# Kernel tuning notes

Measured on AMD Instinct MI355X. Metric: run time of the kernel, lower is better.

## Reference

```python
import jax, jax.numpy as jnp
import numpy as np

B, S, D, H, G, K = 4, 4096, 1024, 16, 4, 3
DG = D // G   # group channels = 256
DH = D // H   # head channels = 64


def setup_inputs() -> dict:
    key = jax.random.key(0)
    ks = jax.random.split(key, 8)
    def w(k, shape, std=0.02):
        return jax.random.normal(k, shape, jnp.float32) * std
    return {
        "x": jax.random.normal(ks[0], (B, S, D), jnp.float32),
        "Wq": w(ks[1], (D, D)), "bq": jnp.zeros((D,), jnp.float32),
        "Wk": w(ks[2], (D, D)), "bk": jnp.zeros((D,), jnp.float32),
        "Wv": w(ks[3], (D, D)), "bv": jnp.zeros((D,), jnp.float32),
        "Wo": w(ks[4], (D, D)), "bo": jnp.zeros((D,), jnp.float32),
        "Woff1": w(ks[5], (DG, DG, K)), "boff1": jnp.zeros((DG,), jnp.float32),
        "Woff2": w(ks[6], (DG,)),
        "bias_table": w(ks[7], (1, 1, S)),
    }


def reference(x, Wq, bq, Wk, bk, Wv, bv, Wo, bo, Woff1, boff1, Woff2, bias_table):
    bsz, seq, d = x.shape
    scale = d ** (-0.5)
    xc = jnp.transpose(x, (0, 2, 1))  # [B, D, S]

    # 1x1 conv projections == channel GEMMs
    q = jnp.einsum('oc,bcs->bos', Wq, xc) + bq[None, :, None]  # [B, D, S]

    # group: [B*G, DG, S]
    gq = q.reshape(bsz * G, DG, seq)
    # offset head: conv1d(k=3, pad=1) -> conv1d(k=1, no bias) -> [B*G, S]
    h = jax.lax.conv_general_dilated(
        gq, Woff1, window_strides=(1,), padding=((K // 2, K // 2),),
        dimension_numbers=('NCH', 'OIH', 'NCH')) + boff1[None, :, None]
    offset = jnp.einsum('c,bcs->bs', Woff2, h)
    offset = jnp.tanh(offset) * K  # offset_range_factor = kernel

    gx = xc.reshape(bsz * G, DG, seq)  # grouped x

    # faithful replication of _grid_sample_1d: F.grid_sample on feats [N,C,S,1]
    # with grid (x = vgrid_scaled -> width dim of size 1, y = 0 -> height dim of
    # size S), bilinear, zero padding, align_corners=False.
    grid = jnp.arange(seq, dtype=x.dtype)[None, :]
    vgrid_scaled = 2.0 * (grid + offset) / max(seq - 1, 1) - 1.0  # [B*G, S]
    ix = vgrid_scaled / 2.0                 # unnormalized width coord (W=1)
    wx = jnp.clip(1.0 - jnp.abs(ix), 0.0, 1.0)  # bilinear weight on width idx 0
    iy = (seq - 1) / 2.0                    # unnormalized height coord for y=0
    y0 = int(np.floor(iy)); y1 = min(y0 + 1, seq - 1)
    wy1 = float(iy - y0); wy0 = 1.0 - wy1
    feat_c = wy0 * gx[:, :, y0] + wy1 * gx[:, :, y1]  # [B*G, DG]
    x_sampled = feat_c[:, :, None] * wx[:, None, :]   # [B*G, DG, S]
    xs = x_sampled.reshape(bsz, d, seq)               # ungroup -> [B, D, S]

    k = jnp.einsum('oc,bcs->bos', Wk, xs) + bk[None, :, None]
    v = jnp.einsum('oc,bcs->bos', Wv, xs) + bv[None, :, None]

    qh = q.reshape(bsz * H, DH, seq)
    kh = k.reshape(bsz * H, DH, seq)
    vh = v.reshape(bsz * H, DH, seq) + bias_table[:, :, :seq]

    # channel attention: contract over sequence dim (as in the original einsum)
    scores = jnp.einsum('bis,bjs->bij', qh, kh) * scale  # [B*H, DH, DH]
    attn = jax.nn.softmax(scores, axis=-1)
    out = jnp.einsum('bij,bjs->bis', attn, vh)           # [B*H, DH, S]
    out = out.reshape(bsz, d, seq).transpose(0, 2, 1)     # [B, S, D]
    return jnp.einsum('bsd,od->bso', out, Wo) + bo
```

## Files before the change

kernel.cpp:

```cpp
#include <hip/hip_runtime.h>
#include <math.h>

#define BB 4
#define SS 4096
#define DD 1024
#define HH 16
#define GG 4
#define KK 3
#define DG 256
#define DH 64
#define CH 32
#define NCH (SS / CH)

enum : size_t {
  OFF_WEFF  = 0,
  OFF_OFFC  = 1024,
  OFF_WEQ   = 1280,
  OFF_WX    = 13568,
  OFF_XWP   = 79104,
  OFF_XW    = 2700544,
  OFF_XS    = 2716928,
  OFF_SW    = 2721024,
  OFF_FEAT  = 2721280,
  OFF_KF    = 2725376,
  OFF_VF    = 2741760,
  OFF_QW    = 2758144,
  OFF_QS    = 2774528,
  OFF_AV    = 2778624,
  OFF_AB    = 2795008,
  OFF_C2    = 2799104,
  OFF_WAV   = 2803200,
  OFF_WOSUM = 2819584,
  WS_FLOATS = 2820608
};

__device__ __forceinline__ float wred_sum(float v) {
#pragma unroll
  for (int o = 32; o > 0; o >>= 1) v += __shfl_xor(v, o, 64);
  return v;
}
__device__ __forceinline__ float wred_max(float v) {
#pragma unroll
  for (int o = 32; o > 0; o >>= 1) v = fmaxf(v, __shfl_xor(v, o, 64));
  return v;
}

__global__ void k_pre1(const float* __restrict__ Woff1, const float* __restrict__ Woff2,
                       const float* __restrict__ x, const float* __restrict__ Wo,
                       float* __restrict__ ws) {
  const int t = threadIdx.x;
  const int lane = t & 63;
  if (blockIdx.x < 192) {
    const int widx = (blockIdx.x * 256 + t) >> 6;
    const int i = widx / 3, kk = widx - 3 * i;
    float a = 0.f;
#pragma unroll
    for (int u = 0; u < 4; ++u) {
      const int cc = lane + 64 * u;
      a += Woff2[cc] * Woff1[(size_t)(cc * DG + i) * KK + kk];
    }
    a = wred_sum(a);
    if (lane == 0) ws[OFF_WEFF + widx] = a;
  } else if (blockIdx.x < 208) {
    const int gid = (blockIdx.x - 192) * 256 + t;
    const int b = gid >> 10, c = gid & 1023;
    ws[OFF_FEAT + gid] = 0.5f * (x[((size_t)b * SS + 2047) * DD + c] +
                                 x[((size_t)b * SS + 2048) * DD + c]);
  } else {
    const int o = ((blockIdx.x - 208) * 256 + t) >> 6;
    const float4* wo = (const float4*)(Wo + (size_t)o * DD);
    float v = 0.f;
#pragma unroll
    for (int it = 0; it < 4; ++it) {
      const float4 a = wo[lane + 64 * it];
      v += a.x + a.y + a.z + a.w;
    }
    v = wred_sum(v);
    if (lane == 0) ws[OFF_WOSUM + o] = v;
  }
}

__global__ void k_pre2(const float* __restrict__ Wq, const float* __restrict__ bq,
                       const float* __restrict__ Woff2, const float* __restrict__ boff1,
                       float* __restrict__ ws) {
  const float* Weff = ws + OFF_WEFF;
  const int t = threadIdx.x;
  const int lane = t & 63;
  if (blockIdx.x < 192) {
    const int j = blockIdx.x >> 4;
    const int c0 = (blockIdx.x & 15) * 64;
    const int g = j / 3, kk = j - 3 * g;
    const int q = t >> 6;
    float a = 0.f;
#pragma unroll 4
    for (int ii = 0; ii < 64; ++ii) {
      const int i = q * 64 + ii;
      a += Weff[i * KK + kk] * Wq[(size_t)(g * DG + i) * DD + c0 + lane];
    }
    __shared__ float red[4][64];
    red[q][lane] = a;
    __syncthreads();
    if (q == 0) {
      const float v = red[0][lane] + red[1][lane] + red[2][lane] + red[3][lane];
      ws[OFF_WEQ + (size_t)j * DD + c0 + lane] = v;
    }
  } else {
    if (t >= 64) return;
    float beff = 0.f;
#pragma unroll
    for (int u = 0; u < 4; ++u) {
      const int cc = lane + 64 * u;
      beff += Woff2[cc] * boff1[cc];
    }
    beff = wred_sum(beff);
#pragma unroll
    for (int g = 0; g < 4; ++g) {
      float a = 0.f;
#pragma unroll
      for (int u = 0; u < 4; ++u) {
        const int i = lane + 64 * u;
        a += (Weff[i * 3 + 0] + Weff[i * 3 + 1] + Weff[i * 3 + 2]) * bq[g * DG + i];
      }
      a = wred_sum(a);
      if (lane == 0) ws[OFF_OFFC + g] = a + beff;
    }
  }
}

__global__ __launch_bounds__(256, 2) void k_main(const float* __restrict__ x,
                                                 float* __restrict__ ws) {
  const int b = blockIdx.x >> 7;
  const int chunk = blockIdx.x & 127;
  const int s0 = chunk * CH;
  const int t = threadIdx.x;
  const int lane = t & 63;
  const int wvid = t >> 6;
  __shared__ float zsh[CH + 2][12];
  __shared__ float wxs[4][CH];

  const float* weq = ws + OFF_WEQ;
  float4 w[12][4];
#pragma unroll
  for (int j = 0; j < 12; ++j)
#pragma unroll
    for (int it = 0; it < 4; ++it)
      w[j][it] = *(const float4*)(weq + (size_t)j * DD + 4 * (lane + 64 * it));

  for (int r = wvid; r < CH + 2; r += 4) {
    const int s = s0 - 1 + r;
    if (s < 0 || s >= SS) continue;
    const float4* xr = (const float4*)(x + (size_t)(b * SS + s) * DD);
    float4 xv[4];
#pragma unroll
    for (int it = 0; it < 4; ++it) xv[it] = xr[lane + 64 * it];
    float acc[12];
#pragma unroll
    for (int j = 0; j < 12; ++j) {
      float a = 0.f;
#pragma unroll
      for (int it = 0; it < 4; ++it)
        a += xv[it].x * w[j][it].x + xv[it].y * w[j][it].y +
             xv[it].z * w[j][it].z + xv[it].w * w[j][it].w;
      acc[j] = a;
    }
#pragma unroll
    for (int j = 0; j < 12; ++j) acc[j] = wred_sum(acc[j]);
    if (lane == 0) {
#pragma unroll
      for (int j = 0; j < 12; ++j) zsh[r][j] = acc[j];
    }
  }
  __syncthreads();

  if (t < CH) {
    const int s = s0 + t;
#pragma unroll
    for (int g = 0; g < 4; ++g) {
      float off = ws[OFF_OFFC + g];
      if (s > 0)      off += zsh[t][g * 3 + 0];
      off += zsh[t + 1][g * 3 + 1];
      if (s < SS - 1) off += zsh[t + 2][g * 3 + 2];
      off = tanhf(off) * (float)KK;
      const float vg = 2.0f * ((float)s + off) / (float)(SS - 1) - 1.0f;
      float wvv = 1.0f - fabsf(0.5f * vg);
      wvv = fminf(fmaxf(wvv, 0.0f), 1.0f);
      wxs[g][t] = wvv;
      ws[OFF_WX + (size_t)(b * GG + g) * SS + s] = wvv;
    }
  }
  __syncthreads();

  float4 aw[5] = {};
#pragma unroll 4
  for (int si = 0; si < CH; ++si) {
    const int s = s0 + si;
    const float4 f = *(const float4*)(x + (size_t)(b * SS + s) * DD + 4 * t);
    const float w0 = wxs[0][si], w1 = wxs[1][si], w2 = wxs[2][si], w3 = wxs[3][si];
    aw[0].x += f.x * w0; aw[0].y += f.y * w0; aw[0].z += f.z * w0; aw[0].w += f.w * w0;
    aw[1].x += f.x * w1; aw[1].y += f.y * w1; aw[1].z += f.z * w1; aw[1].w += f.w * w1;
    aw[2].x += f.x * w2; aw[2].y += f.y * w2; aw[2].z += f.z * w2; aw[2].w += f.w * w2;
    aw[3].x += f.x * w3; aw[3].y += f.y * w3; aw[3].z += f.z * w3; aw[3].w += f.w * w3;
    aw[4].x += f.x; aw[4].y += f.y; aw[4].z += f.z; aw[4].w += f.w;
  }
#pragma unroll
  for (int slot = 0; slot < 5; ++slot)
    *(float4*)(ws + OFF_XWP + (((size_t)(b * 5 + slot) * NCH + chunk) * DD) + 4 * t) = aw[slot];
}

__global__ void k_xw_red(float* __restrict__ ws) {
  const int t = threadIdx.x;
  const int lane = t & 63;
  if (blockIdx.x < 320) {
    const int b = blockIdx.x / 80;
    const int rem = blockIdx.x - b * 80;
    const int slot = rem >> 4;
    const int c0 = (rem & 15) * 64;
    const int q = t >> 6;
    const float* base = ws + OFF_XWP + (size_t)(b * 5 + slot) * NCH * DD;
    float a = 0.f;
#pragma unroll 4
    for (int ii = 0; ii < 32; ++ii) {
      const int ch = q * 32 + ii;
      a += base[(size_t)ch * DD + c0 + lane];
    }
    __shared__ float red[4][64];
    red[q][lane] = a;
    __syncthreads();
    if (q == 0) {
      const float v = red[0][lane] + red[1][lane] + red[2][lane] + red[3][lane];
      if (slot < 4) ws[OFF_XW + ((size_t)(b * GG + slot)) * DD + c0 + lane] = v;
      else          ws[OFF_XS + (size_t)b * DD + c0 + lane] = v;
    }
  } else {
    const int w = blockIdx.x - 320;
    const float* wx = ws + OFF_WX + (size_t)w * SS;
    float a = 0.f;
#pragma unroll 4
    for (int it = 0; it < 16; ++it) a += wx[t + 256 * it];
    a = wred_sum(a);
    __shared__ float red[4];
    if (lane == 0) red[t >> 6] = a;
    __syncthreads();
    if (t == 0) ws[OFF_SW + w] = red[0] + red[1] + red[2] + red[3];
  }
}

__global__ void k_dots(const float* __restrict__ Wq, const float* __restrict__ bq,
                       const float* __restrict__ Wk, const float* __restrict__ Wv,
                       float* __restrict__ ws) {
  const int t = threadIdx.x;
  const int lane = t & 63;
  if (blockIdx.x < 1024) {
    const int widx = blockIdx.x * 4 + (t >> 6);
    const int g = widx >> 10, o = widx & 1023;
    const float4 ak = ((const float4*)(Wk + (size_t)o * DD + g * DG))[lane];
    const float4 avv = ((const float4*)(Wv + (size_t)o * DD + g * DG))[lane];
    float kk[4], vv[4];
#pragma unroll
    for (int b = 0; b < 4; ++b) {
      const float4 f = ((const float4*)(ws + OFF_FEAT + (size_t)b * DD + g * DG))[lane];
      kk[b] = ak.x * f.x + ak.y * f.y + ak.z * f.z + ak.w * f.w;
      vv[b] = avv.x * f.x + avv.y * f.y + avv.z * f.z + avv.w * f.w;
    }
#pragma unroll
    for (int b = 0; b < 4; ++b) { kk[b] = wred_sum(kk[b]); vv[b] = wred_sum(vv[b]); }
    if (lane == 0) {
#pragma unroll
      for (int b = 0; b < 4; ++b) {
        ws[OFF_KF + ((size_t)(b * GG + g)) * DD + o] = kk[b];
        ws[OFF_VF + ((size_t)(b * GG + g)) * DD + o] = vv[b];
      }
    }
  } else {
    const int widx = (blockIdx.x - 1024) * 4 + (t >> 6);
    const int b = widx >> 10, I = widx & 1023;
    const float4* wq = (const float4*)(Wq + (size_t)I * DD);
    float4 a[4];
#pragma unroll
    for (int it = 0; it < 4; ++it) a[it] = wq[lane + 64 * it];
    float acc[5] = {0.f, 0.f, 0.f, 0.f, 0.f};
#pragma unroll
    for (int g = 0; g < 4; ++g) {
      const float4* xw = (const float4*)(ws + OFF_XW + (size_t)(b * GG + g) * DD);
#pragma unroll
      for (int it = 0; it < 4; ++it) {
        const float4 c = xw[lane + 64 * it];
        acc[g] += a[it].x * c.x + a[it].y * c.y + a[it].z * c.z + a[it].w * c.w;
      }
    }
    const float4* xs = (const float4*)(ws + OFF_XS + (size_t)b * DD);
#pragma unroll
    for (int it = 0; it < 4; ++it) {
      const float4 c = xs[lane + 64 * it];
      acc[4] += a[it].x * c.x + a[it].y * c.y + a[it].z * c.z + a[it].w * c.w;
    }
#pragma unroll
    for (int u = 0; u < 5; ++u) acc[u] = wred_sum(acc[u]);
    if (lane == 0) {
      const float bqi = bq[I];
#pragma unroll
      for (int g = 0; g < 4; ++g)
        ws[OFF_QW + ((size_t)(b * DD + I)) * 4 + g] = acc[g] + bqi * ws[OFF_SW + b * GG + g];
      ws[OFF_QS + (size_t)b * DD + I] = acc[4] + (float)SS * bqi;
    }
  }
}

__global__ void k_attn(const float* __restrict__ bk, const float* __restrict__ bv,
                       float* __restrict__ ws) {
  const int gid = blockIdx.x * blockDim.x + threadIdx.x;
  const int lane = gid & 63;
  const int w = gid >> 6;
  if (w >= BB * DD) return;
  const int b = w >> 10, d = w & 1023;
  const int hh = d >> 6;
  const int J = (hh << 6) | lane;
  const float* Qw = ws + OFF_QW + (size_t)w * 4;
  const float q0 = Qw[0], q1 = Qw[1], q2 = Qw[2], q3 = Qw[3];
  const float qs = ws[OFF_QS + w];
  const float* Kf = ws + OFF_KF + (size_t)b * GG * DD;
  float sc = q0 * Kf[0 * DD + J] + q1 * Kf[1 * DD + J] +
             q2 * Kf[2 * DD + J] + q3 * Kf[3 * DD + J] + bk[J] * qs;
  sc *= 0.03125f;
  const float m = wred_max(sc);
  const float e = expf(sc - m);
  const float sum = wred_sum(e);
  const float attn = e / sum;
  const float* Vf = ws + OFF_VF + (size_t)b * GG * DD;
#pragma unroll
  for (int g = 0; g < 4; ++g) {
    const float av = wred_sum(attn * Vf[(size_t)g * DD + J]);
    if (lane == 0) ws[OFF_AV + (size_t)w * 4 + g] = av;
  }
  const float ab = wred_sum(attn * bv[J]);
  if (lane == 0) ws[OFF_AB + w] = ab;
}

__global__ void k_wav(const float* __restrict__ Wo, const float* __restrict__ bo,
                      float* __restrict__ ws) {
  const int gid = blockIdx.x * blockDim.x + threadIdx.x;
  const int lane = gid & 63;
  const int w = gid >> 6;
  if (w >= BB * DD) return;
  const int b = w >> 10, o = w & 1023;
  float acc0 = 0, acc1 = 0, acc2 = 0, acc3 = 0, acc4 = 0;
  const float4* wo4 = (const float4*)(Wo + (size_t)o * DD);
  const float* AV = ws + OFF_AV + (size_t)b * DD * 4;
  const float* Ab = ws + OFF_AB + (size_t)b * DD;
#pragma unroll
  for (int it = 0; it < 4; ++it) {
    const int d4 = lane + 64 * it;
    const float4 wv = wo4[d4];
    const float4 a0 = *(const float4*)(AV + (size_t)(4 * d4 + 0) * 4);
    const float4 a1 = *(const float4*)(AV + (size_t)(4 * d4 + 1) * 4);
    const float4 a2 = *(const float4*)(AV + (size_t)(4 * d4 + 2) * 4);
    const float4 a3 = *(const float4*)(AV + (size_t)(4 * d4 + 3) * 4);
    acc0 += wv.x * a0.x + wv.y * a1.x + wv.z * a2.x + wv.w * a3.x;
    acc1 += wv.x * a0.y + wv.y * a1.y + wv.z * a2.y + wv.w * a3.y;
    acc2 += wv.x * a0.z + wv.y * a1.z + wv.z * a2.z + wv.w * a3.z;
    acc3 += wv.x * a0.w + wv.y * a1.w + wv.z * a2.w + wv.w * a3.w;
    const float4 abv = *(const float4*)(Ab + 4 * d4);
    acc4 += wv.x * abv.x + wv.y * abv.y + wv.z * abv.z + wv.w * abv.w;
  }
  acc0 = wred_sum(acc0); acc1 = wred_sum(acc1); acc2 = wred_sum(acc2);
  acc3 = wred_sum(acc3); acc4 = wred_sum(acc4);
  if (lane == 0) {
    float* WAV = ws + OFF_WAV + (size_t)w * 4;
    WAV[0] = acc0; WAV[1] = acc1; WAV[2] = acc2; WAV[3] = acc3;
    ws[OFF_C2 + w] = acc4 + bo[o];
  }
}

__global__ __launch_bounds__(256) void k_out(const float* __restrict__ btab,
                                             const float* __restrict__ ws,
                                             float* __restrict__ out) {
  const int b = blockIdx.x >> 8;
  const int ch = blockIdx.x & 255;
  const int t = threadIdx.x;
  const int o0 = 4 * t;
  float4 wav[4];
#pragma unroll
  for (int io = 0; io < 4; ++io)
    wav[io] = *(const float4*)(ws + OFF_WAV + (size_t)(b * DD + o0 + io) * 4);
  const float4 c24 = *(const float4*)(ws + OFF_C2 + (size_t)b * DD + o0);
  const float4 wos4 = *(const float4*)(ws + OFF_WOSUM + o0);
  const float* wx = ws + OFF_WX;
  const int s0 = ch * 16;
#pragma unroll 2
  for (int si = 0; si < 16; ++si) {
    const int s = s0 + si;
    const float w0 = wx[(size_t)(b * GG + 0) * SS + s];
    const float w1 = wx[(size_t)(b * GG + 1) * SS + s];
    const float w2 = wx[(size_t)(b * GG + 2) * SS + s];
    const float w3 = wx[(size_t)(b * GG + 3) * SS + s];
    const float bt = btab[s];
    float4 val;
    val.x = c24.x + bt * wos4.x + w0 * wav[0].x + w1 * wav[0].y + w2 * wav[0].z + w3 * wav[0].w;
    val.y = c24.y + bt * wos4.y + w0 * wav[1].x + w1 * wav[1].y + w2 * wav[1].z + w3 * wav[1].w;
    val.z = c24.z + bt * wos4.z + w0 * wav[2].x + w1 * wav[2].y + w2 * wav[2].z + w3 * wav[2].w;
    val.w = c24.w + bt * wos4.w + w0 * wav[3].x + w1 * wav[3].y + w2 * wav[3].z + w3 * wav[3].w;
    *(float4*)(out + (size_t)(b * SS + s) * DD + o0) = val;
  }
}

extern "C" void kernel_launch(void* const* d_in, const int* in_sizes, int n_in,
                              void* d_out, int out_size, void* d_ws, size_t ws_size,
                              hipStream_t stream) {
  const float* x     = (const float*)d_in[0];
  const float* Wq    = (const float*)d_in[1];
  const float* bq    = (const float*)d_in[2];
  const float* Wk    = (const float*)d_in[3];
  const float* bk    = (const float*)d_in[4];
  const float* Wv    = (const float*)d_in[5];
  const float* bv    = (const float*)d_in[6];
  const float* Wo    = (const float*)d_in[7];
  const float* bo    = (const float*)d_in[8];
  const float* Woff1 = (const float*)d_in[9];
  const float* boff1 = (const float*)d_in[10];
  const float* Woff2 = (const float*)d_in[11];
  const float* btab  = (const float*)d_in[12];
  float* ws  = (float*)d_ws;
  float* out = (float*)d_out;

  k_pre1<<<464, 256, 0, stream>>>(Woff1, Woff2, x, Wo, ws);
  k_pre2<<<193, 256, 0, stream>>>(Wq, bq, Woff2, boff1, ws);
  k_main<<<512, 256, 0, stream>>>(x, ws);
  k_xw_red<<<336, 256, 0, stream>>>(ws);
  k_dots<<<2048, 256, 0, stream>>>(Wq, bq, Wk, Wv, ws);
  k_attn<<<1024, 256, 0, stream>>>(bk, bv, ws);
  k_wav<<<1024, 256, 0, stream>>>(Wo, bo, ws);
  k_out<<<1024, 256, 0, stream>>>(btab, ws, out);
}
```

Before: 217.4 us.

## Split offset projection from weighted reduction and fuse dots with attention

The old fused main kernel computed the 12 offset projections per row inside each sequence chunk, recomputing the halo rows. It is now split into a grid-stride projection kernel that writes a per-row buffer, and a separate weighted-sum kernel with a smaller chunk size that gives more blocks. The K/V feature dots move into k_pre2, and the Q dots are fused with the softmax attention into one kernel, which removes a launch and an intermediate buffer. In exchange, x is read twice across kernels and the partial-sum buffer doubles in size.

```diff
diff --git a/kernel.cpp b/kernel.cpp
--- a/kernel.cpp
+++ b/kernel.cpp
@@ -9,29 +9,28 @@
 #define KK 3
 #define DG 256
 #define DH 64
-#define CH 32
+#define CH 16
 #define NCH (SS / CH)
 
 enum : size_t {
   OFF_WEFF  = 0,
   OFF_OFFC  = 1024,
   OFF_WEQ   = 1280,
-  OFF_WX    = 13568,
-  OFF_XWP   = 79104,
-  OFF_XW    = 2700544,
-  OFF_XS    = 2716928,
-  OFF_SW    = 2721024,
-  OFF_FEAT  = 2721280,
-  OFF_KF    = 2725376,
-  OFF_VF    = 2741760,
-  OFF_QW    = 2758144,
-  OFF_QS    = 2774528,
-  OFF_AV    = 2778624,
-  OFF_AB    = 2795008,
-  OFF_C2    = 2799104,
-  OFF_WAV   = 2803200,
-  OFF_WOSUM = 2819584,
-  WS_FLOATS = 2820608
+  OFF_ZT    = 13568,
+  OFF_WX    = 210176,
+  OFF_XWP   = 275712,
+  OFF_XW    = 5518592,
+  OFF_XS    = 5534976,
+  OFF_SW    = 5539072,
+  OFF_FEAT  = 5539328,
+  OFF_KF    = 5543424,
+  OFF_VF    = 5559808,
+  OFF_AV    = 5576192,
+  OFF_AB    = 5592576,
+  OFF_C2    = 5596672,
+  OFF_WAV   = 5600768,
+  OFF_WOSUM = 5617152,
+  WS_FLOATS = 5618176
 };
 
 __device__ __forceinline__ float wred_sum(float v) {
@@ -82,6 +81,7 @@
 
 __global__ void k_pre2(const float* __restrict__ Wq, const float* __restrict__ bq,
                        const float* __restrict__ Woff2, const float* __restrict__ boff1,
+                       const float* __restrict__ Wk, const float* __restrict__ Wv,
                        float* __restrict__ ws) {
   const float* Weff = ws + OFF_WEFF;
   const int t = threadIdx.x;
@@ -104,7 +104,7 @@
       const float v = red[0][lane] + red[1][lane] + red[2][lane] + red[3][lane];
       ws[OFF_WEQ + (size_t)j * DD + c0 + lane] = v;
     }
-  } else {
+  } else if (blockIdx.x == 192) {
     if (t >= 64) return;
     float beff = 0.f;
 #pragma unroll
@@ -124,32 +124,44 @@
       a = wred_sum(a);
       if (lane == 0) ws[OFF_OFFC + g] = a + beff;
     }
-  }
-}
-
-__global__ __launch_bounds__(256, 2) void k_main(const float* __restrict__ x,
-                                                 float* __restrict__ ws) {
-  const int b = blockIdx.x >> 7;
-  const int chunk = blockIdx.x & 127;
-  const int s0 = chunk * CH;
-  const int t = threadIdx.x;
-  const int lane = t & 63;
-  const int wvid = t >> 6;
-  __shared__ float zsh[CH + 2][12];
-  __shared__ float wxs[4][CH];
-
-  const float* weq = ws + OFF_WEQ;
+  } else {
+    const int widx = (blockIdx.x - 193) * 4 + (t >> 6);
+    const int g = widx >> 10, o = widx & 1023;
+    const float4 ak = ((const float4*)(Wk + (size_t)o * DD + g * DG))[lane];
+    const float4 avv = ((const float4*)(Wv + (size_t)o * DD + g * DG))[lane];
+    float kk[4], vv[4];
+#pragma unroll
+    for (int b = 0; b < 4; ++b) {
+      const float4 f = ((const float4*)(ws + OFF_FEAT + (size_t)b * DD + g * DG))[lane];
+      kk[b] = ak.x * f.x + ak.y * f.y + ak.z * f.z + ak.w * f.w;
+      vv[b] = avv.x * f.x + avv.y * f.y + avv.z * f.z + avv.w * f.w;
+    }
+#pragma unroll
+    for (int b = 0; b < 4; ++b) { kk[b] = wred_sum(kk[b]); vv[b] = wred_sum(vv[b]); }
+    if (lane == 0) {
+#pragma unroll
+      for (int b = 0; b < 4; ++b) {
+        ws[OFF_KF + ((size_t)(b * GG + g)) * DD + o] = kk[b];
+        ws[OFF_VF + ((size_t)(b * GG + g)) * DD + o] = vv[b];
+      }
+    }
+  }
+}
+
+__global__ __launch_bounds__(256, 2) void k_z(const float* __restrict__ x,
+                                              const float* __restrict__ weq,
+                                              float* __restrict__ zt) {
+  const int lane = threadIdx.x & 63;
+  const int wave = (blockIdx.x * blockDim.x + threadIdx.x) >> 6;
+  const int nwaves = (gridDim.x * blockDim.x) >> 6;
   float4 w[12][4];
 #pragma unroll
   for (int j = 0; j < 12; ++j)
 #pragma unroll
     for (int it = 0; it < 4; ++it)
       w[j][it] = *(const float4*)(weq + (size_t)j * DD + 4 * (lane + 64 * it));
-
-  for (int r = wvid; r < CH + 2; r += 4) {
-    const int s = s0 - 1 + r;
-    if (s < 0 || s >= SS) continue;
-    const float4* xr = (const float4*)(x + (size_t)(b * SS + s) * DD);
+  for (int row = wave; row < BB * SS; row += nwaves) {
+    const float4* xr = (const float4*)(x + (size_t)row * DD);
     float4 xv[4];
 #pragma unroll
     for (int it = 0; it < 4; ++it) xv[it] = xr[lane + 64 * it];
@@ -167,26 +179,34 @@
     for (int j = 0; j < 12; ++j) acc[j] = wred_sum(acc[j]);
     if (lane == 0) {
 #pragma unroll
-      for (int j = 0; j < 12; ++j) zsh[r][j] = acc[j];
-    }
-  }
-  __syncthreads();
-
-  if (t < CH) {
-    const int s = s0 + t;
-#pragma unroll
-    for (int g = 0; g < 4; ++g) {
-      float off = ws[OFF_OFFC + g];
-      if (s > 0)      off += zsh[t][g * 3 + 0];
-      off += zsh[t + 1][g * 3 + 1];
-      if (s < SS - 1) off += zsh[t + 2][g * 3 + 2];
-      off = tanhf(off) * (float)KK;
-      const float vg = 2.0f * ((float)s + off) / (float)(SS - 1) - 1.0f;
-      float wvv = 1.0f - fabsf(0.5f * vg);
-      wvv = fminf(fmaxf(wvv, 0.0f), 1.0f);
-      wxs[g][t] = wvv;
-      ws[OFF_WX + (size_t)(b * GG + g) * SS + s] = wvv;
-    }
+      for (int j = 0; j < 12; ++j) zt[(size_t)row * 12 + j] = acc[j];
+    }
+  }
+}
+
+__global__ __launch_bounds__(256) void k_xw(const float* __restrict__ x,
+                                            float* __restrict__ ws) {
+  const int b = blockIdx.x >> 8;
+  const int chunk = blockIdx.x & 255;
+  const int s0 = chunk * CH;
+  const int t = threadIdx.x;
+  __shared__ float wxs[4][CH];
+
+  if (t < 64) {
+    const int g = t >> 4, si = t & 15;
+    const int s = s0 + si;
+    const size_t row = (size_t)b * SS + s;
+    const float* zt = ws + OFF_ZT;
+    float off = ws[OFF_OFFC + g];
+    if (s > 0)      off += zt[(row - 1) * 12 + g * 3 + 0];
+    off += zt[row * 12 + g * 3 + 1];
+    if (s < SS - 1) off += zt[(row + 1) * 12 + g * 3 + 2];
+    off = tanhf(off) * (float)KK;
+    const float vg = 2.0f * ((float)s + off) / (float)(SS - 1) - 1.0f;
+    float wvv = 1.0f - fabsf(0.5f * vg);
+    wvv = fminf(fmaxf(wvv, 0.0f), 1.0f);
+    wxs[g][si] = wvv;
+    ws[OFF_WX + (size_t)(b * GG + g) * SS + s] = wvv;
   }
   __syncthreads();
 
@@ -207,29 +227,27 @@
     *(float4*)(ws + OFF_XWP + (((size_t)(b * 5 + slot) * NCH + chunk) * DD) + 4 * t) = aw[slot];
 }
 
-__global__ void k_xw_red(float* __restrict__ ws) {
+__global__ void k_red(float* __restrict__ ws) {
   const int t = threadIdx.x;
   const int lane = t & 63;
+  const int wvid = t >> 6;
+  __shared__ float red[4][64];
   if (blockIdx.x < 320) {
-    const int b = blockIdx.x / 80;
-    const int rem = blockIdx.x - b * 80;
+    const int rb = blockIdx.x / 80;
+    const int rem = blockIdx.x - rb * 80;
     const int slot = rem >> 4;
-    const int c0 = (rem & 15) * 64;
-    const int q = t >> 6;
-    const float* base = ws + OFF_XWP + (size_t)(b * 5 + slot) * NCH * DD;
+    const int c = (rem & 15) * 64 + lane;
+    const float* base = ws + OFF_XWP + (size_t)(rb * 5 + slot) * NCH * DD;
     float a = 0.f;
-#pragma unroll 4
-    for (int ii = 0; ii < 32; ++ii) {
-      const int ch = q * 32 + ii;
-      a += base[(size_t)ch * DD + c0 + lane];
-    }
-    __shared__ float red[4][64];
-    red[q][lane] = a;
+#pragma unroll 8
+    for (int ii = 0; ii < 64; ++ii)
+      a += base[(size_t)(wvid * 64 + ii) * DD + c];
+    red[wvid][lane] = a;
     __syncthreads();
-    if (q == 0) {
+    if (wvid == 0) {
       const float v = red[0][lane] + red[1][lane] + red[2][lane] + red[3][lane];
-      if (slot < 4) ws[OFF_XW + ((size_t)(b * GG + slot)) * DD + c0 + lane] = v;
-      else          ws[OFF_XS + (size_t)b * DD + c0 + lane] = v;
+      if (slot < 4) ws[OFF_XW + ((size_t)(rb * GG + slot)) * DD + c] = v;
+      else          ws[OFF_XS + (size_t)rb * DD + c] = v;
     }
   } else {
     const int w = blockIdx.x - 320;
@@ -238,87 +256,49 @@
 #pragma unroll 4
     for (int it = 0; it < 16; ++it) a += wx[t + 256 * it];
     a = wred_sum(a);
-    __shared__ float red[4];
-    if (lane == 0) red[t >> 6] = a;
+    if (lane == 0) red[0][wvid] = a;
     __syncthreads();
-    if (t == 0) ws[OFF_SW + w] = red[0] + red[1] + red[2] + red[3];
-  }
-}
-
-__global__ void k_dots(const float* __restrict__ Wq, const float* __restrict__ bq,
-                       const float* __restrict__ Wk, const float* __restrict__ Wv,
-                       float* __restrict__ ws) {
+    if (t == 0) ws[OFF_SW + w] = red[0][0] + red[0][1] + red[0][2] + red[0][3];
+  }
+}
+
+__global__ void k_mid(const float* __restrict__ Wq, const float* __restrict__ bq,
+                      const float* __restrict__ bk, const float* __restrict__ bv,
+                      float* __restrict__ ws) {
   const int t = threadIdx.x;
   const int lane = t & 63;
-  if (blockIdx.x < 1024) {
-    const int widx = blockIdx.x * 4 + (t >> 6);
-    const int g = widx >> 10, o = widx & 1023;
-    const float4 ak = ((const float4*)(Wk + (size_t)o * DD + g * DG))[lane];
-    const float4 avv = ((const float4*)(Wv + (size_t)o * DD + g * DG))[lane];
-    float kk[4], vv[4];
-#pragma unroll
-    for (int b = 0; b < 4; ++b) {
-      const float4 f = ((const float4*)(ws + OFF_FEAT + (size_t)b * DD + g * DG))[lane];
-      kk[b] = ak.x * f.x + ak.y * f.y + ak.z * f.z + ak.w * f.w;
-      vv[b] = avv.x * f.x + avv.y * f.y + avv.z * f.z + avv.w * f.w;
-    }
-#pragma unroll
-    for (int b = 0; b < 4; ++b) { kk[b] = wred_sum(kk[b]); vv[b] = wred_sum(vv[b]); }
-    if (lane == 0) {
-#pragma unroll
-      for (int b = 0; b < 4; ++b) {
-        ws[OFF_KF + ((size_t)(b * GG + g)) * DD + o] = kk[b];
-        ws[OFF_VF + ((size_t)(b * GG + g)) * DD + o] = vv[b];
-      }
-    }
-  } else {
-    const int widx = (blockIdx.x - 1024) * 4 + (t >> 6);
-    const int b = widx >> 10, I = widx & 1023;
-    const float4* wq = (const float4*)(Wq + (size_t)I * DD);
-    float4 a[4];
-#pragma unroll
-    for (int it = 0; it < 4; ++it) a[it] = wq[lane + 64 * it];
-    float acc[5] = {0.f, 0.f, 0.f, 0.f, 0.f};
-#pragma unroll
-    for (int g = 0; g < 4; ++g) {
-      const float4* xw = (const float4*)(ws + OFF_XW + (size_t)(b * GG + g) * DD);
-#pragma unroll
-      for (int it = 0; it < 4; ++it) {
-        const float4 c = xw[lane + 64 * it];
-        acc[g] += a[it].x * c.x + a[it].y * c.y + a[it].z * c.z + a[it].w * c.w;
-      }
-    }
-    const float4* xs = (const float4*)(ws + OFF_XS + (size_t)b * DD);
+  const int wave = blockIdx.x * 4 + (t >> 6);
+  const int ab_ = wave >> 10, I = wave & 1023;
+  const float4* wq = (const float4*)(Wq + (size_t)I * DD);
+  float4 a[4];
+#pragma unroll
+  for (int it = 0; it < 4; ++it) a[it] = wq[lane + 64 * it];
+  float acc[5] = {0.f, 0.f, 0.f, 0.f, 0.f};
+#pragma unroll
+  for (int g = 0; g < 4; ++g) {
+    const float4* xw = (const float4*)(ws + OFF_XW + (size_t)(ab_ * GG + g) * DD);
 #pragma unroll
     for (int it = 0; it < 4; ++it) {
-      const float4 c = xs[lane + 64 * it];
-      acc[4] += a[it].x * c.x + a[it].y * c.y + a[it].z * c.z + a[it].w * c.w;
-    }
-#pragma unroll
-    for (int u = 0; u < 5; ++u) acc[u] = wred_sum(acc[u]);
-    if (lane == 0) {
-      const float bqi = bq[I];
-#pragma unroll
-      for (int g = 0; g < 4; ++g)
-        ws[OFF_QW + ((size_t)(b * DD + I)) * 4 + g] = acc[g] + bqi * ws[OFF_SW + b * GG + g];
-      ws[OFF_QS + (size_t)b * DD + I] = acc[4] + (float)SS * bqi;
-    }
-  }
-}
-
-__global__ void k_attn(const float* __restrict__ bk, const float* __restrict__ bv,
-                       float* __restrict__ ws) {
-  const int gid = blockIdx.x * blockDim.x + threadIdx.x;
-  const int lane = gid & 63;
-  const int w = gid >> 6;
-  if (w >= BB * DD) return;
-  const int b = w >> 10, d = w & 1023;
-  const int hh = d >> 6;
-  const int J = (hh << 6) | lane;
-  const float* Qw = ws + OFF_QW + (size_t)w * 4;
-  const float q0 = Qw[0], q1 = Qw[1], q2 = Qw[2], q3 = Qw[3];
-  const float qs = ws[OFF_QS + w];
-  const float* Kf = ws + OFF_KF + (size_t)b * GG * DD;
+      const float4 c = xw[lane + 64 * it];
+      acc[g] += a[it].x * c.x + a[it].y * c.y + a[it].z * c.z + a[it].w * c.w;
+    }
+  }
+  const float4* xs = (const float4*)(ws + OFF_XS + (size_t)ab_ * DD);
+#pragma unroll
+  for (int it = 0; it < 4; ++it) {
+    const float4 c = xs[lane + 64 * it];
+    acc[4] += a[it].x * c.x + a[it].y * c.y + a[it].z * c.z + a[it].w * c.w;
+  }
+#pragma unroll
+  for (int u = 0; u < 5; ++u) acc[u] = wred_sum(acc[u]);
+  const float bqi = bq[I];
+  const float q0 = acc[0] + bqi * ws[OFF_SW + ab_ * GG + 0];
+  const float q1 = acc[1] + bqi * ws[OFF_SW + ab_ * GG + 1];
+  const float q2 = acc[2] + bqi * ws[OFF_SW + ab_ * GG + 2];
+  const float q3 = acc[3] + bqi * ws[OFF_SW + ab_ * GG + 3];
+  const float qs = acc[4] + (float)SS * bqi;
+  const int J = (I & ~63) | lane;
+  const float* Kf = ws + OFF_KF + (size_t)ab_ * GG * DD;
   float sc = q0 * Kf[0 * DD + J] + q1 * Kf[1 * DD + J] +
              q2 * Kf[2 * DD + J] + q3 * Kf[3 * DD + J] + bk[J] * qs;
   sc *= 0.03125f;
@@ -326,14 +306,14 @@
   const float e = expf(sc - m);
   const float sum = wred_sum(e);
   const float attn = e / sum;
-  const float* Vf = ws + OFF_VF + (size_t)b * GG * DD;
+  const float* Vf = ws + OFF_VF + (size_t)ab_ * GG * DD;
 #pragma unroll
   for (int g = 0; g < 4; ++g) {
     const float av = wred_sum(attn * Vf[(size_t)g * DD + J]);
-    if (lane == 0) ws[OFF_AV + (size_t)w * 4 + g] = av;
-  }
-  const float ab = wred_sum(attn * bv[J]);
-  if (lane == 0) ws[OFF_AB + w] = ab;
+    if (lane == 0) ws[OFF_AV + (size_t)wave * 4 + g] = av;
+  }
+  const float abv = wred_sum(attn * bv[J]);
+  if (lane == 0) ws[OFF_AB + wave] = abv;
 }
 
 __global__ void k_wav(const float* __restrict__ Wo, const float* __restrict__ bo,
@@ -385,9 +365,9 @@
   const float4 c24 = *(const float4*)(ws + OFF_C2 + (size_t)b * DD + o0);
   const float4 wos4 = *(const float4*)(ws + OFF_WOSUM + o0);
   const float* wx = ws + OFF_WX;
-  const int s0 = ch * 16;
+  const int s0 = ch * CH;
 #pragma unroll 2
-  for (int si = 0; si < 16; ++si) {
+  for (int si = 0; si < CH; ++si) {
     const int s = s0 + si;
     const float w0 = wx[(size_t)(b * GG + 0) * SS + s];
     const float w1 = wx[(size_t)(b * GG + 1) * SS + s];
@@ -423,11 +403,11 @@
   float* out = (float*)d_out;
 
   k_pre1<<<464, 256, 0, stream>>>(Woff1, Woff2, x, Wo, ws);
-  k_pre2<<<193, 256, 0, stream>>>(Wq, bq, Woff2, boff1, ws);
-  k_main<<<512, 256, 0, stream>>>(x, ws);
-  k_xw_red<<<336, 256, 0, stream>>>(ws);
-  k_dots<<<2048, 256, 0, stream>>>(Wq, bq, Wk, Wv, ws);
-  k_attn<<<1024, 256, 0, stream>>>(bk, bv, ws);
+  k_pre2<<<1217, 256, 0, stream>>>(Wq, bq, Woff2, boff1, Wk, Wv, ws);
+  k_z<<<512, 256, 0, stream>>>(x, ws + OFF_WEQ, ws + OFF_ZT);
+  k_xw<<<1024, 256, 0, stream>>>(x, ws);
+  k_red<<<336, 256, 0, stream>>>(ws);
+  k_mid<<<1024, 256, 0, stream>>>(Wq, bq, bk, bv, ws);
   k_wav<<<1024, 256, 0, stream>>>(Wo, bo, ws);
   k_out<<<1024, 256, 0, stream>>>(btab, ws, out);
 }
```

Result: no change. 215.1 us (-1.0%).
